# Kernel optimization log

Hardware: AMD Instinct MI355X
Metric: run time of the kernel (lower is better)

The kernel has to match this reference:

```python
import jax, jax.numpy as jnp
import numpy as np

EMBED_DIM = 1024
NUM_HEADS = 16
HEAD_DIM = EMBED_DIM // NUM_HEADS
SCALE = HEAD_DIM ** -0.5
B, S = 2, 2048


def setup_inputs() -> dict:
    key = jax.random.key(0)
    ks = jax.random.split(key, 11)
    lim = 1.0 / np.sqrt(EMBED_DIM)
    def lin(kw, kb):
        W = jax.random.uniform(kw, (EMBED_DIM, EMBED_DIM), jnp.float32, -lim, lim)
        b = jax.random.uniform(kb, (EMBED_DIM,), jnp.float32, -lim, lim)
        return W, b
    Wq, bq = lin(ks[0], ks[1])
    Wk, bk = lin(ks[2], ks[3])
    Wv, bv = lin(ks[4], ks[5])
    Wo, bo = lin(ks[6], ks[7])
    query = jax.random.normal(ks[8], (B, S, EMBED_DIM), jnp.float32)
    key_t = jax.random.normal(ks[9], (B, S, EMBED_DIM), jnp.float32)
    value = jax.random.normal(ks[10], (B, S, EMBED_DIM), jnp.float32)
    return {"query": query, "key": key_t, "value": value,
            "Wq": Wq, "bq": bq, "Wk": Wk, "bk": bk,
            "Wv": Wv, "bv": bv, "Wo": Wo, "bo": bo}


def reference(query, key, value, Wq, bq, Wk, bk, Wv, bv, Wo, bo):
    # 'flash' path with attn_mask=None == full softmax attention (chunking is
    # only an execution schedule; per-chunk softmax is over the full key axis).
    b, s, _ = query.shape
    def heads(x, W, bias):
        y = x @ W.T + bias                      # [b, s, E]
        return y.reshape(b, s, NUM_HEADS, HEAD_DIM).transpose(0, 2, 1, 3)  # [b, h, s, d]
    q = heads(query, Wq, bq)
    k = heads(key, Wk, bk)
    v = heads(value, Wv, bv)
    scores = jnp.einsum('bhqd,bhkd->bhqk', q, k) * SCALE
    attn = jax.nn.softmax(scores, axis=-1)
    out = jnp.einsum('bhqk,bhkd->bhqd', attn, v)
    out = out.transpose(0, 2, 1, 3).reshape(b, s, EMBED_DIM)
    return out @ Wo.T + bo
```

## Files before the change

kernel.cpp:

```cpp
#include <hip/hip_runtime.h>

typedef unsigned short u16;
typedef unsigned int u32;
typedef __attribute__((ext_vector_type(8))) __bf16 bf16x8;
typedef __attribute__((ext_vector_type(4))) float f32x4;
typedef __attribute__((ext_vector_type(4))) unsigned short u16x4;
typedef __attribute__((ext_vector_type(8))) unsigned short u16x8;
typedef __attribute__((ext_vector_type(4))) unsigned int u32x4;

#define DEV static __device__ __forceinline__

DEV void async_copy16(const void* g, void* l) {
  __builtin_amdgcn_global_load_lds((const __attribute__((address_space(1))) void*)g,
                                   (__attribute__((address_space(3))) void*)l, 16, 0, 0);
}
DEV float b2f(u16 s) { union { unsigned u; float f; } v; v.u = ((unsigned)s) << 16; return v.f; }
DEV u16 f2b(float f) {
  union { float f; unsigned u; } v; v.f = f;
  unsigned r = v.u + 0x7FFFu + ((v.u >> 16) & 1u);
  return (u16)(r >> 16);
}
DEV u32 pack2bf(float a, float b) {
  u32 ua = __float_as_uint(a) + 0x8000u;
  u32 ub = __float_as_uint(b) + 0x8000u;
  return __builtin_amdgcn_perm(ub, ua, 0x07060302u);
}

#define MFMA(a, b, c) __builtin_amdgcn_mfma_f32_16x16x32_bf16((a), (b), (c), 0, 0, 0)

__global__ void detect_dtype(const unsigned* __restrict__ q, int* __restrict__ flag) {
  const int lane = threadIdx.x;
  const unsigned w = q[lane];
  const unsigned e = (w >> 7) & 0xFFu;
  const bool inr = (e >= 100u && e <= 132u);
  const unsigned long long m = __ballot(inr);
  if (lane == 0) flag[0] = (__popcll(m) >= 48) ? 1 : 0;
}

__global__ void convert_inputs(
    const void* s0, const void* s1, const void* s2,
    const void* s3, const void* s4, const void* s5, const void* s6,
    const void* s7, const void* s8, const void* s9, const void* s10,
    u16* __restrict__ d0, u16* __restrict__ d1, u16* __restrict__ d2,
    u16* __restrict__ d3, u16* __restrict__ d4, u16* __restrict__ d5, u16* __restrict__ d6,
    float* __restrict__ e7, float* __restrict__ e8, float* __restrict__ e9, float* __restrict__ e10,
    const int* __restrict__ flag)
{
  const int bi = blockIdx.y;
  const void* src = nullptr; u16* db = nullptr; float* df = nullptr; int n = 0;
  switch (bi) {
    case 0:  src = s0;  db = d0; n = 4194304; break;
    case 1:  src = s1;  db = d1; n = 4194304; break;
    case 2:  src = s2;  db = d2; n = 4194304; break;
    case 3:  src = s3;  db = d3; n = 1048576; break;
    case 4:  src = s4;  db = d4; n = 1048576; break;
    case 5:  src = s5;  db = d5; n = 1048576; break;
    case 6:  src = s6;  db = d6; n = 1048576; break;
    case 7:  src = s7;  df = e7; n = 1024; break;
    case 8:  src = s8;  df = e8; n = 1024; break;
    case 9:  src = s9;  df = e9; n = 1024; break;
    default: src = s10; df = e10; n = 1024; break;
  }
  const int isbf = flag[0];
  const int stride = gridDim.x * 256 * 8;
  for (int i = (blockIdx.x * 256 + threadIdx.x) * 8; i < n; i += stride) {
    if (db) {
      u16x8 v;
      if (isbf) {
        v = *(const u16x8*)((const u16*)src + i);
      } else {
        const float* sf = (const float*)src;
#pragma unroll
        for (int j = 0; j < 8; ++j) v[j] = f2b(sf[i + j]);
      }
      *(u16x8*)(db + i) = v;
    } else {
#pragma unroll
      for (int j = 0; j < 8; ++j) {
        float x = isbf ? b2f(((const u16*)src)[i + j]) : ((const float*)src)[i + j];
        df[i + j] = x;
      }
    }
  }
}

__global__ void gemm_qkv(const u16* __restrict__ X0, const u16* __restrict__ X1, const u16* __restrict__ X2,
                         const u16* __restrict__ W0, const u16* __restrict__ W1, const u16* __restrict__ W2,
                         const float* __restrict__ B0, const float* __restrict__ B1, const float* __restrict__ B2,
                         u16* __restrict__ Y0, u16* __restrict__ Y1, u16* __restrict__ Y2,
                         float* __restrict__ Yf, const int* __restrict__ flag, int mode0)
{
  __shared__ __align__(16) u16 smem[17408];

  const int z = blockIdx.z;
  const u16* X  = (z == 0) ? X0 : ((z == 1) ? X1 : X2);
  const u16* W  = (z == 0) ? W0 : ((z == 1) ? W1 : W2);
  const float* Bi = (z == 0) ? B0 : ((z == 1) ? B1 : B2);
  u16* Y        = (z == 0) ? Y0 : ((z == 1) ? Y1 : Y2);
  const int mode = mode0 ? mode0 : z;
  const int outbf = flag[0];

  const int t = threadIdx.x, wave = t >> 6, lane = t & 63;
  const int lane15 = lane & 15, quad = lane >> 4;

  const int L = blockIdx.y * 8 + blockIdx.x;
  const int wrk = (L & 7) * 32 + (L >> 3);
  const int m0 = (wrk >> 3) * 128, n0 = (wrk & 7) * 128;

  const u16* gA = X + (size_t)(m0 + wave * 16 + (lane >> 2)) * 1024 + (lane & 3) * 8;
  const u16* gB = W + (size_t)(n0 + wave * 16 + (lane >> 2)) * 1024 + (lane & 3) * 8;

  f32x4 acc[4][4];
#pragma unroll
  for (int i = 0; i < 4; ++i)
#pragma unroll
    for (int j = 0; j < 4; ++j) acc[i][j] = (f32x4){0.f, 0.f, 0.f, 0.f};

  const int wr = wave >> 1, wc = wave & 1;

  u16* lA0 = smem + wave * 512;
  u16* lB0 = smem + 4096 + wave * 512;
  u16* lA1 = smem + 8192 + wave * 512;
  u16* lB1 = smem + 12288 + wave * 512;

  auto stage = [&](u16* lA, u16* lB) {
    async_copy16(gA, lA);
    async_copy16(gA + 64 * 1024, lA + 64 * 32);
    async_copy16(gB, lB);
    async_copy16(gB + 64 * 1024, lB + 64 * 32);
    gA += 32; gB += 32;
  };
  auto compute = [&](const u16* As_, const u16* Bs_) {
    bf16x8 af[4], bfv[4];
#pragma unroll
    for (int mt = 0; mt < 4; ++mt)
      af[mt] = *(const bf16x8*)&As_[(wr * 64 + mt * 16 + lane15) * 32 + quad * 8];
#pragma unroll
    for (int nt = 0; nt < 4; ++nt)
      bfv[nt] = *(const bf16x8*)&Bs_[(wc * 64 + nt * 16 + lane15) * 32 + quad * 8];
#pragma unroll
    for (int mt = 0; mt < 4; ++mt)
#pragma unroll
      for (int nt = 0; nt < 4; ++nt)
        acc[mt][nt] = MFMA(af[mt], bfv[nt], acc[mt][nt]);
  };

  stage(lA0, lB0);
  __syncthreads();

  for (int k0 = 0; k0 < 1024; k0 += 64) {
    if (k0 + 32 < 1024) stage(lA1, lB1);
    compute(smem, smem + 4096);
    __syncthreads();
    if (k0 + 64 < 1024) stage(lA0, lB0);
    compute(smem + 8192, smem + 12288);
    __syncthreads();
  }

  const float qscale = 0.125f * 1.44269504088896340736f;

  if (mode == 2) {
    u16* T2 = smem;
#pragma unroll
    for (int mt = 0; mt < 4; ++mt) {
      const int sl_base = wr * 64 + mt * 16 + quad * 4;
#pragma unroll
      for (int nt = 0; nt < 4; ++nt) {
        const int nn = wc * 64 + nt * 16 + lane15;
        const float bias_v = Bi[n0 + nn];
#pragma unroll
        for (int r = 0; r < 4; ++r) {
          const int sl = sl_base + r;
          const int sp = ((sl & 15) << 3) | (sl >> 4);
          T2[nn * 136 + sp] = f2b(acc[mt][nt][r] + bias_v);
        }
      }
    }
    __syncthreads();
    const size_t grow0 = (size_t)(m0 >> 11) * 1024 + n0;
    const int col0 = m0 & 2047;
#pragma unroll
    for (int i = 0; i < 8; ++i) {
      const int id = i * 256 + t;
      const int row = id >> 4, ch = id & 15;
      *(u16x8*)&Y[(grow0 + row) * 2048 + col0 + ch * 8] = *(const u16x8*)&T2[row * 136 + ch * 8];
    }
    return;
  }

#pragma unroll
  for (int mt = 0; mt < 4; ++mt) {
    const int m_base = m0 + wr * 64 + mt * 16 + quad * 4;
#pragma unroll
    for (int nt = 0; nt < 4; ++nt) {
      const int n = n0 + wc * 64 + nt * 16 + lane15;
      const float bias_v = Bi[n];
#pragma unroll
      for (int r = 0; r < 4; ++r) {
        const int m = m_base + r;
        float v = acc[mt][nt][r] + bias_v;
        if (mode == 0) v *= qscale;
        if (mode == 3) {
          if (outbf) Y[(size_t)m * 1024 + n] = f2b(v);
          else       Yf[(size_t)m * 1024 + n] = v;
        } else {
          size_t addr = (((size_t)(m >> 11) * 16 + (n >> 6)) * 2048 + (size_t)(m & 2047)) * 64 + (n & 63);
          Y[addr] = f2b(v);
        }
      }
    }
  }
}

__global__ __launch_bounds__(256, 2) void flash_attn(const u16* __restrict__ Qs, const u16* __restrict__ Ks,
                                                     const u16* __restrict__ Vt, u16* __restrict__ AO)
{
  __shared__ __align__(16) u16 smem[32768];
  u16* Kt = smem;
  u16* Vs = smem + 8192;

  const int t = threadIdx.x, wave = t >> 6, lane = t & 63;
  const int lane15 = lane & 15, quad = lane >> 4;
  const int l7 = lane15 & 7;

  const int Lb = blockIdx.y * 16 + blockIdx.x;
  const int wrk = (Lb & 7) * 64 + (Lb >> 3);
  const int bh = wrk >> 4;
  const int q0 = (wrk & 15) * 128;
  u16* Pw = smem + 16384 + wave * 4096;

  const u16* Qb = Qs + ((size_t)bh * 2048 + q0) * 64;
  const u16* Kb = Ks + (size_t)bh * 2048 * 64;
  const u16* Vb = Vt + (size_t)bh * 64 * 2048;

  const int krow = lane >> 3;
  const int kchunk = (lane & 7) ^ (krow & 7);
  const int vrow = lane >> 4;
  const int vchunk = (lane & 15) ^ (((wave & 1) << 2) + vrow);

#pragma unroll
  for (int r = 0; r < 4; ++r)
    async_copy16(Qb + (size_t)(r * 32 + wave * 8 + krow) * 64 + kchunk * 8,
                 &Kt[(r * 32 + wave * 8) * 64]);
  __syncthreads();
  bf16x8 aq[2][2];
#pragma unroll
  for (int mt = 0; mt < 2; ++mt)
#pragma unroll
    for (int ks = 0; ks < 2; ++ks)
      aq[mt][ks] = *(const bf16x8*)&Kt[(wave * 32 + mt * 16 + lane15) * 64 + ((ks * 4 + quad) ^ l7) * 8];
  __syncthreads();

  f32x4 acc_o[2][4], acc_l[2];
#pragma unroll
  for (int mt = 0; mt < 2; ++mt) {
    acc_l[mt] = (f32x4){0.f, 0.f, 0.f, 0.f};
#pragma unroll
    for (int i = 0; i < 4; ++i) acc_o[mt][i] = (f32x4){0.f, 0.f, 0.f, 0.f};
  }

  u16x8 ou;
#pragma unroll
  for (int j = 0; j < 8; ++j) ou[j] = 0x3F80;
  const bf16x8 ones = __builtin_bit_cast(bf16x8, ou);

  for (int kt = 0; kt < 16; ++kt) {
#pragma unroll
    for (int r = 0; r < 4; ++r)
      async_copy16(Kb + (size_t)(kt * 128 + r * 32 + wave * 8 + krow) * 64 + kchunk * 8,
                   &Kt[(r * 32 + wave * 8) * 64]);
#pragma unroll
    for (int r = 0; r < 4; ++r)
      async_copy16(Vb + (size_t)(r * 16 + wave * 4 + vrow) * 2048 + kt * 128 + vchunk * 8,
                   &Vs[(r * 16 + wave * 4) * 128]);
    __syncthreads();

    f32x4 s[2][8];
#pragma unroll
    for (int mt = 0; mt < 2; ++mt)
#pragma unroll
      for (int nt = 0; nt < 8; ++nt) s[mt][nt] = (f32x4){0.f, 0.f, 0.f, 0.f};
#pragma unroll
    for (int ks = 0; ks < 2; ++ks) {
      bf16x8 bk[8];
#pragma unroll
      for (int nt = 0; nt < 8; ++nt)
        bk[nt] = *(const bf16x8*)&Kt[(nt * 16 + lane15) * 64 + ((ks * 4 + quad) ^ l7) * 8];
#pragma unroll
      for (int mt = 0; mt < 2; ++mt)
#pragma unroll
        for (int nt = 0; nt < 8; ++nt)
          s[mt][nt] = MFMA(aq[mt][ks], bk[nt], s[mt][nt]);
    }

#pragma unroll
    for (int mt = 0; mt < 2; ++mt)
#pragma unroll
      for (int rg = 0; rg < 4; ++rg) {
        u32x4 w;
#pragma unroll
        for (int j = 0; j < 4; ++j)
          w[j] = pack2bf(__builtin_amdgcn_exp2f(s[mt][2 * j][rg]),
                         __builtin_amdgcn_exp2f(s[mt][2 * j + 1][rg]));
        const int r = mt * 16 + quad * 4 + rg;
        *(u32x4*)&Pw[r * 128 + (lane15 ^ (r & 7)) * 8] = w;
      }
    __threadfence_block();

#pragma unroll
    for (int ks2 = 0; ks2 < 4; ++ks2) {
      bf16x8 bv[4], ap[2];
#pragma unroll
      for (int dt = 0; dt < 4; ++dt)
        bv[dt] = *(const bf16x8*)&Vs[(dt * 16 + lane15) * 128 + ((ks2 * 4 + quad) ^ l7) * 8];
#pragma unroll
      for (int mt = 0; mt < 2; ++mt)
        ap[mt] = *(const bf16x8*)&Pw[(mt * 16 + lane15) * 128 + ((ks2 * 4 + quad) ^ l7) * 8];
#pragma unroll
      for (int mt = 0; mt < 2; ++mt) {
#pragma unroll
        for (int dt = 0; dt < 4; ++dt)
          acc_o[mt][dt] = MFMA(ap[mt], bv[dt], acc_o[mt][dt]);
        acc_l[mt] = MFMA(ap[mt], ones, acc_l[mt]);
      }
    }
    __syncthreads();
  }

  float rinv[2][4];
#pragma unroll
  for (int mt = 0; mt < 2; ++mt)
#pragma unroll
    for (int rg = 0; rg < 4; ++rg) rinv[mt][rg] = 1.0f / acc_l[mt][rg];

  u16* T = smem;
#pragma unroll
  for (int mt = 0; mt < 2; ++mt)
#pragma unroll
    for (int dt = 0; dt < 4; ++dt)
#pragma unroll
      for (int rg = 0; rg < 4; ++rg)
        T[(wave * 32 + mt * 16 + quad * 4 + rg) * 72 + dt * 16 + lane15] =
            f2b(acc_o[mt][dt][rg] * rinv[mt][rg]);
  __syncthreads();

  const int b = bh >> 4, h = bh & 15;
#pragma unroll
  for (int i = 0; i < 4; ++i) {
    const int id = i * 256 + t;
    const int row = id >> 3, ch = id & 7;
    *(u16x8*)&AO[((size_t)b * 2048 + q0 + row) * 1024 + h * 64 + ch * 8] =
        *(const u16x8*)&T[row * 72 + ch * 8];
  }
}

extern "C" void kernel_launch(void* const* d_in, const int* in_sizes, int n_in,
                              void* d_out, int out_size, void* d_ws, size_t ws_size,
                              hipStream_t stream)
{
  const void* query = d_in[0];
  const void* key_  = d_in[1];
  const void* value = d_in[2];
  const void* Wq = d_in[3]; const void* bq = d_in[4];
  const void* Wk = d_in[5]; const void* bk = d_in[6];
  const void* Wv = d_in[7]; const void* bv = d_in[8];
  const void* Wo = d_in[9]; const void* bo = d_in[10];

  u16* ws = (u16*)d_ws;
  u16* Qs  = ws;
  u16* Ks  = Qs + 4194304;
  u16* Vt  = Ks + 4194304;
  u16* AO  = Vt + 4194304;
  u16* Xq  = AO + 4194304;
  u16* Xk  = Xq + 4194304;
  u16* Xv  = Xk + 4194304;
  u16* Wqc = Xv + 4194304;
  u16* Wkc = Wqc + 1048576;
  u16* Wvc = Wkc + 1048576;
  u16* Woc = Wvc + 1048576;
  float* Bc = (float*)(Woc + 1048576);
  int* flag = (int*)(Bc + 4096);

  detect_dtype<<<1, 64, 0, stream>>>((const unsigned*)query, flag);
  convert_inputs<<<dim3(128, 11), 256, 0, stream>>>(
      query, key_, value, Wq, Wk, Wv, Wo, bq, bk, bv, bo,
      Xq, Xk, Xv, Wqc, Wkc, Wvc, Woc,
      Bc, Bc + 1024, Bc + 2048, Bc + 3072, flag);

  gemm_qkv<<<dim3(8, 32, 3), 256, 0, stream>>>(Xq, Xk, Xv, Wqc, Wkc, Wvc,
                                               Bc, Bc + 1024, Bc + 2048,
                                               Qs, Ks, Vt, nullptr, flag, 0);
  flash_attn<<<dim3(16, 32), 256, 0, stream>>>(Qs, Ks, Vt, AO);
  gemm_qkv<<<dim3(8, 32, 1), 256, 0, stream>>>(AO, AO, AO, Woc, Woc, Woc,
                                               Bc + 3072, Bc + 3072, Bc + 3072,
                                               (u16*)d_out, (u16*)d_out, (u16*)d_out,
                                               (float*)d_out, flag, 3);
}
```

Before: 223.4 us.

## Register-prefetch next K/V tile in attention and raise priority around MFMA blocks

The attention loop now loads the next K/V tile from global memory into registers right after the barrier, then writes them into LDS at the top of the following iteration. This replaces the direct async global-to-LDS copies and lets global latency overlap with the current tile's compute. s_setprio is also raised around the MFMA clusters in both the projection GEMM and the attention kernel, so matrix work gets issue priority. The cost is extra VGPRs for the staged tiles, which may reduce occupancy.

```diff
diff --git a/kernel.cpp b/kernel.cpp
--- a/kernel.cpp
+++ b/kernel.cpp
@@ -138,11 +138,13 @@
 #pragma unroll
     for (int nt = 0; nt < 4; ++nt)
       bfv[nt] = *(const bf16x8*)&Bs_[(wc * 64 + nt * 16 + lane15) * 32 + quad * 8];
+    __builtin_amdgcn_s_setprio(1);
 #pragma unroll
     for (int mt = 0; mt < 4; ++mt)
 #pragma unroll
       for (int nt = 0; nt < 4; ++nt)
         acc[mt][nt] = MFMA(af[mt], bfv[nt], acc[mt][nt]);
+    __builtin_amdgcn_s_setprio(0);
   };
 
   stage(lA0, lB0);
@@ -238,6 +240,27 @@
   const int vrow = lane >> 4;
   const int vchunk = (lane & 15) ^ (((wave & 1) << 2) + vrow);
 
+  const u16* gK0 = Kb + (size_t)(wave * 8 + krow) * 64 + kchunk * 8;
+  const u16* gV0 = Vb + (size_t)(wave * 4 + vrow) * 2048 + vchunk * 8;
+
+  u32x4 kreg[4], vreg[4];
+  auto load_kv = [&](int kt) {
+#pragma unroll
+    for (int r = 0; r < 4; ++r) {
+      kreg[r] = *(const u32x4*)(gK0 + (size_t)(kt * 128 + r * 32) * 64);
+      vreg[r] = *(const u32x4*)(gV0 + (size_t)(r * 16) * 2048 + kt * 128);
+    }
+  };
+  auto write_kv = [&]() {
+#pragma unroll
+    for (int r = 0; r < 4; ++r) {
+      *(u32x4*)&Kt[(r * 32 + wave * 8) * 64 + lane * 8] = kreg[r];
+      *(u32x4*)&Vs[(r * 16 + wave * 4) * 128 + lane * 8] = vreg[r];
+    }
+  };
+
+  load_kv(0);
+
 #pragma unroll
   for (int r = 0; r < 4; ++r)
     async_copy16(Qb + (size_t)(r * 32 + wave * 8 + krow) * 64 + kchunk * 8,
@@ -265,15 +288,9 @@
   const bf16x8 ones = __builtin_bit_cast(bf16x8, ou);
 
   for (int kt = 0; kt < 16; ++kt) {
-#pragma unroll
-    for (int r = 0; r < 4; ++r)
-      async_copy16(Kb + (size_t)(kt * 128 + r * 32 + wave * 8 + krow) * 64 + kchunk * 8,
-                   &Kt[(r * 32 + wave * 8) * 64]);
-#pragma unroll
-    for (int r = 0; r < 4; ++r)
-      async_copy16(Vb + (size_t)(r * 16 + wave * 4 + vrow) * 2048 + kt * 128 + vchunk * 8,
-                   &Vs[(r * 16 + wave * 4) * 128]);
+    write_kv();
     __syncthreads();
+    if (kt + 1 < 16) load_kv(kt + 1);
 
     f32x4 s[2][8];
 #pragma unroll
@@ -286,11 +303,13 @@
 #pragma unroll
       for (int nt = 0; nt < 8; ++nt)
         bk[nt] = *(const bf16x8*)&Kt[(nt * 16 + lane15) * 64 + ((ks * 4 + quad) ^ l7) * 8];
+      __builtin_amdgcn_s_setprio(1);
 #pragma unroll
       for (int mt = 0; mt < 2; ++mt)
 #pragma unroll
         for (int nt = 0; nt < 8; ++nt)
           s[mt][nt] = MFMA(aq[mt][ks], bk[nt], s[mt][nt]);
+      __builtin_amdgcn_s_setprio(0);
     }
 
 #pragma unroll
@@ -316,6 +335,7 @@
 #pragma unroll
       for (int mt = 0; mt < 2; ++mt)
         ap[mt] = *(const bf16x8*)&Pw[(mt * 16 + lane15) * 128 + ((ks2 * 4 + quad) ^ l7) * 8];
+      __builtin_amdgcn_s_setprio(1);
 #pragma unroll
       for (int mt = 0; mt < 2; ++mt) {
 #pragma unroll
@@ -323,6 +343,7 @@
           acc_o[mt][dt] = MFMA(ap[mt], bv[dt], acc_o[mt][dt]);
         acc_l[mt] = MFMA(ap[mt], ones, acc_l[mt]);
       }
+      __builtin_amdgcn_s_setprio(0);
     }
     __syncthreads();
   }
```

Result: no change. 222.8 us (-0.3%).

## Keep softmax probabilities in registers via permlane swaps and raise attention occupancy

Applied to the files above, without the earlier changes.

The attention kernel now computes S^T per 32-key slice and converts the exponentiated scores into the MFMA A-operand layout with permlane32/permlane16 swaps. This removes the per-wave LDS staging buffer for P, which halves shared memory and allows raising launch bounds from 2 to 4 blocks per CU. MFMA sections are wrapped in s_setprio to favour matrix issue, and the mode-2 projection transpose drops its swizzled column index. The risks are more LDS bank conflicts in that transpose store and register pressure at the higher occupancy target.

```diff
diff --git a/kernel.cpp b/kernel.cpp
--- a/kernel.cpp
+++ b/kernel.cpp
@@ -6,6 +6,7 @@
 typedef __attribute__((ext_vector_type(4))) float f32x4;
 typedef __attribute__((ext_vector_type(4))) unsigned short u16x4;
 typedef __attribute__((ext_vector_type(8))) unsigned short u16x8;
+typedef __attribute__((ext_vector_type(2))) unsigned int u32x2;
 typedef __attribute__((ext_vector_type(4))) unsigned int u32x4;
 
 #define DEV static __device__ __forceinline__
@@ -138,11 +139,13 @@
 #pragma unroll
     for (int nt = 0; nt < 4; ++nt)
       bfv[nt] = *(const bf16x8*)&Bs_[(wc * 64 + nt * 16 + lane15) * 32 + quad * 8];
+    __builtin_amdgcn_s_setprio(1);
 #pragma unroll
     for (int mt = 0; mt < 4; ++mt)
 #pragma unroll
       for (int nt = 0; nt < 4; ++nt)
         acc[mt][nt] = MFMA(af[mt], bfv[nt], acc[mt][nt]);
+    __builtin_amdgcn_s_setprio(0);
   };
 
   stage(lA0, lB0);
@@ -171,8 +174,7 @@
 #pragma unroll
         for (int r = 0; r < 4; ++r) {
           const int sl = sl_base + r;
-          const int sp = ((sl & 15) << 3) | (sl >> 4);
-          T2[nn * 136 + sp] = f2b(acc[mt][nt][r] + bias_v);
+          T2[nn * 136 + sl] = f2b(acc[mt][nt][r] + bias_v);
         }
       }
     }
@@ -212,10 +214,10 @@
   }
 }
 
-__global__ __launch_bounds__(256, 2) void flash_attn(const u16* __restrict__ Qs, const u16* __restrict__ Ks,
+__global__ __launch_bounds__(256, 4) void flash_attn(const u16* __restrict__ Qs, const u16* __restrict__ Ks,
                                                      const u16* __restrict__ Vt, u16* __restrict__ AO)
 {
-  __shared__ __align__(16) u16 smem[32768];
+  __shared__ __align__(16) u16 smem[16384];
   u16* Kt = smem;
   u16* Vs = smem + 8192;
 
@@ -227,7 +229,6 @@
   const int wrk = (Lb & 7) * 64 + (Lb >> 3);
   const int bh = wrk >> 4;
   const int q0 = (wrk & 15) * 128;
-  u16* Pw = smem + 16384 + wave * 4096;
 
   const u16* Qb = Qs + ((size_t)bh * 2048 + q0) * 64;
   const u16* Kb = Ks + (size_t)bh * 2048 * 64;
@@ -275,54 +276,61 @@
                    &Vs[(r * 16 + wave * 4) * 128]);
     __syncthreads();
 
-    f32x4 s[2][8];
-#pragma unroll
-    for (int mt = 0; mt < 2; ++mt)
-#pragma unroll
-      for (int nt = 0; nt < 8; ++nt) s[mt][nt] = (f32x4){0.f, 0.f, 0.f, 0.f};
-#pragma unroll
-    for (int ks = 0; ks < 2; ++ks) {
-      bf16x8 bk[8];
-#pragma unroll
-      for (int nt = 0; nt < 8; ++nt)
-        bk[nt] = *(const bf16x8*)&Kt[(nt * 16 + lane15) * 64 + ((ks * 4 + quad) ^ l7) * 8];
+#pragma unroll
+    for (int ks2 = 0; ks2 < 4; ++ks2) {
+      bf16x8 bk[2][2];
+#pragma unroll
+      for (int no = 0; no < 2; ++no)
+#pragma unroll
+        for (int ks = 0; ks < 2; ++ks)
+          bk[no][ks] = *(const bf16x8*)&Kt[((ks2 * 2 + no) * 16 + lane15) * 64 + ((ks * 4 + quad) ^ l7) * 8];
+      f32x4 s2[2][2];
 #pragma unroll
       for (int mt = 0; mt < 2; ++mt)
 #pragma unroll
-        for (int nt = 0; nt < 8; ++nt)
-          s[mt][nt] = MFMA(aq[mt][ks], bk[nt], s[mt][nt]);
-    }
-
-#pragma unroll
-    for (int mt = 0; mt < 2; ++mt)
-#pragma unroll
-      for (int rg = 0; rg < 4; ++rg) {
-        u32x4 w;
-#pragma unroll
-        for (int j = 0; j < 4; ++j)
-          w[j] = pack2bf(__builtin_amdgcn_exp2f(s[mt][2 * j][rg]),
-                         __builtin_amdgcn_exp2f(s[mt][2 * j + 1][rg]));
-        const int r = mt * 16 + quad * 4 + rg;
-        *(u32x4*)&Pw[r * 128 + (lane15 ^ (r & 7)) * 8] = w;
-      }
-    __threadfence_block();
-
-#pragma unroll
-    for (int ks2 = 0; ks2 < 4; ++ks2) {
-      bf16x8 bv[4], ap[2];
+        for (int no = 0; no < 2; ++no) s2[mt][no] = (f32x4){0.f, 0.f, 0.f, 0.f};
+      __builtin_amdgcn_s_setprio(1);
+#pragma unroll
+      for (int mt = 0; mt < 2; ++mt)
+#pragma unroll
+        for (int no = 0; no < 2; ++no)
+#pragma unroll
+          for (int ks = 0; ks < 2; ++ks)
+            s2[mt][no] = MFMA(bk[no][ks], aq[mt][ks], s2[mt][no]);
+      __builtin_amdgcn_s_setprio(0);
+
+      bf16x8 pa[2];
+#pragma unroll
+      for (int mt = 0; mt < 2; ++mt) {
+        float e0[4], e1[4];
+#pragma unroll
+        for (int rg = 0; rg < 4; ++rg) {
+          e0[rg] = __builtin_amdgcn_exp2f(s2[mt][0][rg]);
+          e1[rg] = __builtin_amdgcn_exp2f(s2[mt][1][rg]);
+        }
+        const u32 x0 = pack2bf(e0[0], e0[1]), x1 = pack2bf(e0[2], e0[3]);
+        const u32 y0 = pack2bf(e1[0], e1[1]), y1 = pack2bf(e1[2], e1[3]);
+        const u32x2 rA = __builtin_amdgcn_permlane32_swap(x0, y0, false, false);
+        const u32x2 rB = __builtin_amdgcn_permlane32_swap(x1, y1, false, false);
+        const u32x2 f0 = __builtin_amdgcn_permlane16_swap(rA[0], rA[1], false, false);
+        const u32x2 f1 = __builtin_amdgcn_permlane16_swap(rB[0], rB[1], false, false);
+        const u32x4 paw = (u32x4){f0[0], f1[0], f0[1], f1[1]};
+        pa[mt] = __builtin_bit_cast(bf16x8, paw);
+      }
+
+      bf16x8 bv[4];
 #pragma unroll
       for (int dt = 0; dt < 4; ++dt)
         bv[dt] = *(const bf16x8*)&Vs[(dt * 16 + lane15) * 128 + ((ks2 * 4 + quad) ^ l7) * 8];
-#pragma unroll
-      for (int mt = 0; mt < 2; ++mt)
-        ap[mt] = *(const bf16x8*)&Pw[(mt * 16 + lane15) * 128 + ((ks2 * 4 + quad) ^ l7) * 8];
+      __builtin_amdgcn_s_setprio(1);
 #pragma unroll
       for (int mt = 0; mt < 2; ++mt) {
 #pragma unroll
         for (int dt = 0; dt < 4; ++dt)
-          acc_o[mt][dt] = MFMA(ap[mt], bv[dt], acc_o[mt][dt]);
-        acc_l[mt] = MFMA(ap[mt], ones, acc_l[mt]);
-      }
+          acc_o[mt][dt] = MFMA(pa[mt], bv[dt], acc_o[mt][dt]);
+        acc_l[mt] = MFMA(pa[mt], ones, acc_l[mt]);
+      }
+      __builtin_amdgcn_s_setprio(0);
     }
     __syncthreads();
   }
```

Measured after the change: 221.8 us. About the same (-0.7%).
